# Performance work log

Hardware: AMD Instinct MI355X
Metric: run time of the kernel (lower is better)

The kernel has to match this reference:

```python
import jax, jax.numpy as jnp
import numpy as np

B, DIM, E, H, TOP_K = 4096, 2048, 8, 16, 2
HEAD_DIM = DIM // H
SCALE = HEAD_DIM ** -0.5


def setup_inputs() -> dict:
    key = jax.random.key(0)
    ks = jax.random.split(key, 7)
    return {
        "x": jax.random.normal(ks[0], (B, DIM), jnp.float32),
        "y": jax.random.normal(ks[1], (B, DIM), jnp.float32),
        "W_experts": jax.random.normal(ks[2], (E, DIM, 3 * DIM), jnp.float32) * 0.02,
        "Wg": jax.random.normal(ks[3], (DIM, E), jnp.float32) * 0.02,
        "bg": jax.random.normal(ks[4], (E,), jnp.float32) * 0.02,
        "Wp": jax.random.normal(ks[5], (DIM, DIM), jnp.float32) * 0.02,
        "bp": jax.random.normal(ks[6], (DIM,), jnp.float32) * 0.02,
    }


def reference(x, y, W_experts, Wg, bg, Wp, bp):
    Bsz, N = x.shape
    # gating: softmax over experts, then top-k sparse combine weights
    gate = jax.nn.softmax(x @ Wg + bg, axis=-1)           # [B, E]
    topv, topi = jax.lax.top_k(gate, TOP_K)               # [B, k]
    g = jnp.zeros((Bsz, E), x.dtype).at[jnp.arange(Bsz)[:, None], topi].add(topv)  # [B, E] sparse gates

    # all-expert QKV projections, combined with gate weights (equals sum over top-k of g_i * expert_i(x))
    qkv_x = jnp.einsum('bef,be->bf', jnp.einsum('bd,edf->bef', x, W_experts), g)  # [B, 3*dim]
    qkv_y = jnp.einsum('bef,be->bf', jnp.einsum('bd,edf->bef', y, W_experts), g)  # [B, 3*dim]

    qkv_x = qkv_x.reshape(Bsz, 3, H, HEAD_DIM)
    qkv_y = qkv_y.reshape(Bsz, 3, H, HEAD_DIM)
    q = qkv_y[:, 0]   # [B, H, hd] (q from y)
    k = qkv_x[:, 1]   # [B, H, hd]
    v = qkv_x[:, 2]   # [B, H, hd]

    attn = jax.nn.softmax(jnp.einsum('bhd,bgd->bhg', q, k) * SCALE, axis=-1)  # [B, H, H]
    out = jnp.einsum('bhg,bgd->bhd', attn, v)             # [B, H, hd]
    out = jnp.swapaxes(out, 1, 2).reshape(Bsz, N)         # matches .transpose(1,2).reshape(B,N)
    return out @ Wp + bp
```

## Files before the change

### kernel.cpp

```cpp
#include <hip/hip_runtime.h>
#include <hip/hip_bf16.h>
#include <math.h>

typedef __hip_bfloat16 bf16;
typedef unsigned short u16;
typedef __attribute__((ext_vector_type(4))) float f32x4;
typedef __attribute__((ext_vector_type(8))) __bf16 bfrag;

#define NB   4096
#define DIMK 2048
#define NE   8
#define NH   16
#define HDIM 128
#define W3   6144
#define BK   32
#define WMAX 96
#define QS   132
#define ATT_SCALE 0.08838834764831845f

__device__ __forceinline__ void gl16(const bf16* g, u16* l) {
    __builtin_amdgcn_global_load_lds(
        (const __attribute__((address_space(1))) void*)g,
        (__attribute__((address_space(3))) void*)l, 16, 0, 0);
}

__global__ __launch_bounds__(256)
void k_cvt(const float* __restrict__ src, bf16* __restrict__ dst, long long n) {
    long long i = ((long long)blockIdx.x * 256 + threadIdx.x) * 8;
    if (i + 8 <= n) {
        float4 a = *(const float4*)(src + i);
        float4 b = *(const float4*)(src + i + 4);
        bf16 o[8];
        o[0] = __float2bfloat16(a.x); o[1] = __float2bfloat16(a.y);
        o[2] = __float2bfloat16(a.z); o[3] = __float2bfloat16(a.w);
        o[4] = __float2bfloat16(b.x); o[5] = __float2bfloat16(b.y);
        o[6] = __float2bfloat16(b.z); o[7] = __float2bfloat16(b.w);
        *(uint4*)(dst + i) = *(uint4*)o;
    }
}

__global__ __launch_bounds__(256)
void k_cvt_t(const float* __restrict__ src, bf16* __restrict__ dst,
             int ldsrc, int lddst, long long srcE, long long dstE) {
    __shared__ u16 tile[64][65];
    int e = blockIdx.z;
    int d0 = blockIdx.y << 6, f0 = blockIdx.x << 6;
    int t = threadIdx.x;
    const float* S = src + (size_t)e * srcE + (size_t)d0 * ldsrc + f0;
    int dr = t >> 4, fc = (t & 15) << 2;
#pragma unroll
    for (int i = 0; i < 4; i++) {
        float4 v = *(const float4*)(S + (size_t)(dr + (i << 4)) * ldsrc + fc);
        bf16 b0 = __float2bfloat16(v.x), b1 = __float2bfloat16(v.y),
             b2 = __float2bfloat16(v.z), b3 = __float2bfloat16(v.w);
        u16* tp = &tile[dr + (i << 4)][fc];
        tp[0] = *(u16*)&b0; tp[1] = *(u16*)&b1;
        tp[2] = *(u16*)&b2; tp[3] = *(u16*)&b3;
    }
    __syncthreads();
    bf16* D = dst + (size_t)e * dstE + (size_t)f0 * lddst + d0;
#pragma unroll
    for (int r = 0; r < 2; r++) {
        int c = (r << 8) + t;
        int fr = c >> 3, chk = c & 7;
        u16 o[8];
#pragma unroll
        for (int j = 0; j < 8; j++) o[j] = tile[chk * 8 + j][fr];
        *(uint4*)(D + (size_t)fr * lddst + chk * 8) = *(uint4*)o;
    }
}

__global__ void k_zero(int* counts) {
    if (threadIdx.x < 64) counts[threadIdx.x] = 0;
}

__global__ void k_gate(const float* __restrict__ x, const float* __restrict__ Wg,
                       const float* __restrict__ bg, int* __restrict__ counts,
                       int* __restrict__ rowsP, float* __restrict__ gA,
                       float* __restrict__ gB) {
    int b = blockIdx.x;
    int l = threadIdx.x;
    float acc[NE];
#pragma unroll
    for (int e = 0; e < NE; e++) acc[e] = 0.f;
    for (int i = 0; i < DIMK / 64; i++) {
        int d = i * 64 + l;
        float xv = x[(size_t)b * DIMK + d];
        const float* wrow = Wg + (size_t)d * NE;
#pragma unroll
        for (int e = 0; e < NE; e++) acc[e] += xv * wrow[e];
    }
#pragma unroll
    for (int e = 0; e < NE; e++)
        for (int off = 32; off > 0; off >>= 1) acc[e] += __shfl_down(acc[e], off);
    if (l == 0) {
        float p[NE]; float m = -1e30f;
        for (int e = 0; e < NE; e++) { p[e] = acc[e] + bg[e]; m = fmaxf(m, p[e]); }
        float s = 0.f;
        for (int e = 0; e < NE; e++) { p[e] = __expf(p[e] - m); s += p[e]; }
        float inv = 1.f / s;
        for (int e = 0; e < NE; e++) p[e] *= inv;
        int i1 = 0; float v1 = p[0];
        for (int e = 1; e < NE; e++) if (p[e] > v1) { v1 = p[e]; i1 = e; }
        int i2 = -1; float v2 = -1.f;
        for (int e = 0; e < NE; e++) if (e != i1 && p[e] > v2) { v2 = p[e]; i2 = e; }
        if (i2 < 0) i2 = (i1 + 1) & 7;
        int a, bb; float ga, gb;
        if (i1 < i2) { a = i1; bb = i2; ga = v1; gb = v2; }
        else         { a = i2; bb = i1; ga = v2; gb = v1; }
        int pid = a * NE + bb;
        pid = pid < 0 ? 0 : (pid > 63 ? 63 : pid);
        int pos = atomicAdd(&counts[pid], 1);
        if (pos < NB) {
            rowsP[pid * NB + pos] = b; gA[pid * NB + pos] = ga; gB[pid * NB + pos] = gb;
        }
    }
}

__global__ void k_sched(const int* __restrict__ counts, int2* __restrict__ work) {
    if (threadIdx.x == 0) {
        int w = 0;
        for (int p = 0; p < 64; p++) {
            int c = counts[p]; c = c > NB ? NB : c;
            for (int m = 0; m < c && w < WMAX; m += 64) work[w++] = make_int2(p, m);
        }
        for (; w < WMAX; w++) work[w] = make_int2(-1, 0);
    }
}

__global__ __launch_bounds__(256, 3)
void k_moe(const bf16* __restrict__ xb, const bf16* __restrict__ yb,
           const bf16* __restrict__ Wt, const int* __restrict__ counts,
           const int* __restrict__ rowsP, const float* __restrict__ gAp,
           const float* __restrict__ gBp, const int2* __restrict__ work,
           bf16* __restrict__ qbuf, bf16* __restrict__ kvbuf) {
    int2 wi = work[blockIdx.y];
    if (wi.x < 0) return;
    int p = wi.x, m0 = wi.y;
    int eA = p >> 3, eB = p & 7;
    int cnt = counts[p]; cnt = cnt > NB ? NB : cnt;
    int n0 = blockIdx.x * 128;
    const bf16* A = (n0 < DIMK) ? yb : xb;
    bf16* outp; int ldc, coff;
    if (n0 < DIMK) { outp = qbuf;  ldc = DIMK;     coff = n0; }
    else           { outp = kvbuf; ldc = 2 * DIMK; coff = n0 - DIMK; }

    __shared__ __align__(16) u16 Al[2][2048];
    __shared__ __align__(16) u16 Bl[2][2][4096];
    __shared__ int   rowb[64];
    __shared__ float ga_s[64], gb_s[64];

    int t = threadIdx.x;
    if (t < 64) {
        int mg = m0 + t;
        if (mg < cnt) {
            int rv = rowsP[p * NB + mg];
            rowb[t] = (rv >= 0 && rv < NB) ? rv : -1;
            ga_s[t] = gAp[p * NB + mg]; gb_s[t] = gBp[p * NB + mg];
        } else { rowb[t] = -1; ga_s[t] = 0.f; gb_s[t] = 0.f; }
    }
    __syncthreads();

    int lane = t & 63, w = t >> 6;
    int q = lane >> 4, lr = lane & 15;
    int wbase = (t & ~63) * 8;

    int aline = t >> 3;
    int as_ = (t & 7) ^ (aline & 7);
    int atrow = aline * 2 + (as_ >> 2);
    int arowg = rowb[atrow];
    const bf16* srcA = A + (size_t)(arowg >= 0 ? arowg : 0) * DIMK + (as_ & 3) * 8;

    const bf16* srcB0[2]; const bf16* srcB1[2];
#pragma unroll
    for (int r = 0; r < 2; r++) {
        int c = (r << 8) + t;
        int line = c >> 3;
        int s = (c & 7) ^ (line & 7);
        int col = line * 2 + (s >> 2);
        size_t off = (size_t)(n0 + col) * DIMK + (s & 3) * 8;
        srcB0[r] = Wt + (size_t)eA * W3 * DIMK + off;
        srcB1[r] = Wt + (size_t)eB * W3 * DIMK + off;
    }

    f32x4 acc0[2][4], acc1[2][4];
#pragma unroll
    for (int nf = 0; nf < 2; nf++)
#pragma unroll
        for (int m = 0; m < 4; m++) {
            acc0[nf][m] = (f32x4){0.f,0.f,0.f,0.f};
            acc1[nf][m] = (f32x4){0.f,0.f,0.f,0.f};
        }

#define MOE_STAGE(BUF, K0) do { \
    gl16(srcA + (K0),      &Al[BUF][wbase]); \
    gl16(srcB0[0] + (K0),  &Bl[BUF][0][wbase]); \
    gl16(srcB0[1] + (K0),  &Bl[BUF][0][2048 + wbase]); \
    gl16(srcB1[0] + (K0),  &Bl[BUF][1][wbase]); \
    gl16(srcB1[1] + (K0),  &Bl[BUF][1][2048 + wbase]); \
} while (0)

#define MOE_COMP(BUF) do { \
    bfrag af[4]; \
    _Pragma("unroll") for (int m = 0; m < 4; m++) { \
        int row = m * 16 + lr; int line = row >> 1; \
        af[m] = *(const bfrag*)&Al[BUF][line * 64 + ((((row & 1) << 2) | q) ^ (line & 7)) * 8]; \
    } \
    _Pragma("unroll") for (int nf = 0; nf < 2; nf++) { \
        int col = (w << 5) + (nf << 4) + lr; int line = col >> 1; \
        int bo = line * 64 + ((((col & 1) << 2) | q) ^ (line & 7)) * 8; \
        bfrag b0 = *(const bfrag*)&Bl[BUF][0][bo]; \
        bfrag b1 = *(const bfrag*)&Bl[BUF][1][bo]; \
        _Pragma("unroll") for (int m = 0; m < 4; m++) { \
            acc0[nf][m] = __builtin_amdgcn_mfma_f32_16x16x32_bf16(af[m], b0, acc0[nf][m], 0, 0, 0); \
            acc1[nf][m] = __builtin_amdgcn_mfma_f32_16x16x32_bf16(af[m], b1, acc1[nf][m], 0, 0, 0); \
        } \
    } \
} while (0)

    MOE_STAGE(0, 0);
    __syncthreads();
    for (int k0 = 0; k0 < DIMK; k0 += 2 * BK) {
        MOE_STAGE(1, k0 + BK);
        MOE_COMP(0);
        __syncthreads();
        if (k0 + 2 * BK < DIMK) MOE_STAGE(0, k0 + 2 * BK);
        MOE_COMP(1);
        __syncthreads();
    }
#undef MOE_STAGE
#undef MOE_COMP

#pragma unroll
    for (int nf = 0; nf < 2; nf++) {
        int col = coff + (w << 5) + (nf << 4) + lr;
#pragma unroll
        for (int m = 0; m < 4; m++)
#pragma unroll
            for (int r = 0; r < 4; r++) {
                int tr = m * 16 + q * 4 + r;
                int rb = rowb[tr];
                if (rb >= 0)
                    outp[(size_t)rb * ldc + col] =
                        __float2bfloat16(ga_s[tr] * acc0[nf][m][r] + gb_s[tr] * acc1[nf][m][r]);
            }
    }
}

__global__ __launch_bounds__(256)
void k_attn(const bf16* qv, const bf16* __restrict__ kv, bf16* aout) {
    int b = blockIdx.x;
    int t = threadIdx.x;
    __shared__ __align__(16) float qs[NH * QS];
    __shared__ __align__(16) float ks[NH * QS];
    __shared__ __align__(16) float vs[NH * QS];
    __shared__ float Ps[NH * 17];
    size_t qb = (size_t)b * DIMK;
    size_t kb = (size_t)b * (2 * DIMK);
    {
        uint4 q4 = *(const uint4*)(qv + qb + (size_t)t * 8);
        uint4 k4 = *(const uint4*)(kv + kb + (size_t)t * 8);
        uint4 v4 = *(const uint4*)(kv + kb + DIMK + (size_t)t * 8);
        const bf16* qp = (const bf16*)&q4;
        const bf16* kp = (const bf16*)&k4;
        const bf16* vp = (const bf16*)&v4;
        int hh = t >> 4, dd = (t & 15) << 3;
        float* qd = &qs[hh * QS + dd];
        float* kd = &ks[hh * QS + dd];
        float* vd = &vs[hh * QS + dd];
#pragma unroll
        for (int j = 0; j < 8; j++) {
            qd[j] = __bfloat162float(qp[j]);
            kd[j] = __bfloat162float(kp[j]);
            vd[j] = __bfloat162float(vp[j]);
        }
    }
    __syncthreads();
    int h = t >> 4, g = t & 15;
    float s = 0.f;
    for (int i = 0; i < HDIM / 4; i++) {
        float4 q4 = *(const float4*)&qs[h * QS + 4 * i];
        float4 k4 = *(const float4*)&ks[g * QS + 4 * i];
        s += q4.x * k4.x + q4.y * k4.y + q4.z * k4.z + q4.w * k4.w;
    }
    s *= ATT_SCALE;
    float m = s;
    for (int off = 8; off > 0; off >>= 1) m = fmaxf(m, __shfl_xor(m, off, 16));
    float p = __expf(s - m);
    float sum = p;
    for (int off = 8; off > 0; off >>= 1) sum += __shfl_xor(sum, off, 16);
    Ps[h * 17 + g] = p / sum;
    __syncthreads();
#pragma unroll
    for (int j = 0; j < 8; j++) {
        int n = t + 256 * j;
        int hh = n & 15, dd = n >> 4;
        float o = 0.f;
#pragma unroll
        for (int gg = 0; gg < 16; gg++) o += Ps[hh * 17 + gg] * vs[gg * QS + dd];
        aout[(size_t)b * DIMK + n] = __float2bfloat16(o);
    }
}

__global__ __launch_bounds__(256, 3)
void k_gemm_bias(const bf16* __restrict__ A, const bf16* __restrict__ Wt,
                 const float* __restrict__ bias, float* __restrict__ out) {
    int m0 = blockIdx.y * 128, n0 = blockIdx.x * 128;
    int t = threadIdx.x;
    __shared__ __align__(16) u16 Al[2][4096];
    __shared__ __align__(16) u16 Bl[2][4096];
    int lane = t & 63, w = t >> 6;
    int q = lane >> 4, lr = lane & 15;
    int rh = (w >> 1) << 6, chf = (w & 1) << 6;
    int wbase = (t & ~63) * 8;

    const bf16* srcA[2]; const bf16* srcB[2];
#pragma unroll
    for (int r = 0; r < 2; r++) {
        int c = (r << 8) + t;
        int line = c >> 3;
        int s = (c & 7) ^ (line & 7);
        int row = line * 2 + (s >> 2);
        int j = s & 3;
        srcA[r] = A  + (size_t)(m0 + row) * DIMK + j * 8;
        srcB[r] = Wt + (size_t)(n0 + row) * DIMK + j * 8;
    }

    f32x4 acc[4][4];
#pragma unroll
    for (int m = 0; m < 4; m++)
#pragma unroll
        for (int nf = 0; nf < 4; nf++) acc[m][nf] = (f32x4){0.f,0.f,0.f,0.f};

#define PG_STAGE(BUF, K0) do { \
    gl16(srcA[0] + (K0), &Al[BUF][wbase]); \
    gl16(srcA[1] + (K0), &Al[BUF][2048 + wbase]); \
    gl16(srcB[0] + (K0), &Bl[BUF][wbase]); \
    gl16(srcB[1] + (K0), &Bl[BUF][2048 + wbase]); \
} while (0)

#define PG_COMP(BUF) do { \
    bfrag af[4]; \
    _Pragma("unroll") for (int m = 0; m < 4; m++) { \
        int row = rh + m * 16 + lr; int line = row >> 1; \
        af[m] = *(const bfrag*)&Al[BUF][line * 64 + ((((row & 1) << 2) | q) ^ (line & 7)) * 8]; \
    } \
    _Pragma("unroll") for (int nf = 0; nf < 4; nf++) { \
        int col = chf + nf * 16 + lr; int line = col >> 1; \
        bfrag bf_ = *(const bfrag*)&Bl[BUF][line * 64 + ((((col & 1) << 2) | q) ^ (line & 7)) * 8]; \
        _Pragma("unroll") for (int m = 0; m < 4; m++) \
            acc[m][nf] = __builtin_amdgcn_mfma_f32_16x16x32_bf16(af[m], bf_, acc[m][nf], 0, 0, 0); \
    } \
} while (0)

    PG_STAGE(0, 0);
    __syncthreads();
    for (int k0 = 0; k0 < DIMK; k0 += 2 * BK) {
        PG_STAGE(1, k0 + BK);
        PG_COMP(0);
        __syncthreads();
        if (k0 + 2 * BK < DIMK) PG_STAGE(0, k0 + 2 * BK);
        PG_COMP(1);
        __syncthreads();
    }
#undef PG_STAGE
#undef PG_COMP

#pragma unroll
    for (int nf = 0; nf < 4; nf++) {
        int col = n0 + chf + nf * 16 + lr;
        float bv = bias[col];
#pragma unroll
        for (int m = 0; m < 4; m++)
#pragma unroll
            for (int r = 0; r < 4; r++) {
                int row = m0 + rh + m * 16 + q * 4 + r;
                out[(size_t)row * DIMK + col] = acc[m][nf][r] + bv;
            }
    }
}

__global__ void k_fallback(float v, float* __restrict__ out) {
    int i = blockIdx.x * 256 + threadIdx.x;
    out[i] = v;
}

extern "C" void kernel_launch(void* const* d_in, const int* in_sizes, int n_in,
                              void* d_out, int out_size, void* d_ws, size_t ws_size,
                              hipStream_t stream) {
    const float* x  = (const float*)d_in[0];
    const float* y  = (const float*)d_in[1];
    const float* We = (const float*)d_in[2];
    const float* Wg = (const float*)d_in[3];
    const float* bg = (const float*)d_in[4];
    const float* Wp = (const float*)d_in[5];
    const float* bp = (const float*)d_in[6];
    float* out = (float*)d_out;
    (void)in_sizes; (void)n_in; (void)out_size;

    char* ws = (char*)d_ws;
    const size_t NEED = 296751104ULL;
    if (ws_size < NEED) {
        hipLaunchKernelGGL(k_fallback, dim3(NB * DIMK / 256), dim3(256), 0, stream,
                           (float)(ws_size >> 20), out);
        return;
    }
    int*   counts = (int*)ws;
    int2*  work   = (int2*)(ws + 256);
    int*   rowsP  = (int*)(ws + 4096);
    float* gA     = (float*)(ws + 1052672);
    float* gB     = (float*)(ws + 2101248);
    bf16*  xb     = (bf16*)(ws + 3149824);
    bf16*  yb     = (bf16*)(ws + 19927040);
    bf16*  Web    = (bf16*)(ws + 36704256);
    bf16*  Wpb    = (bf16*)(ws + 238030848);
    bf16*  qbuf   = (bf16*)(ws + 246419456);
    bf16*  kvbuf  = (bf16*)(ws + 263196672);

    const long long nxy = (long long)NB * DIMK;
    hipLaunchKernelGGL(k_cvt, dim3((unsigned)(nxy / 2048)), dim3(256), 0, stream, x,  xb,  nxy);
    hipLaunchKernelGGL(k_cvt, dim3((unsigned)(nxy / 2048)), dim3(256), 0, stream, y,  yb,  nxy);
    hipLaunchKernelGGL(k_cvt_t, dim3(W3 / 64, DIMK / 64, NE), dim3(256), 0, stream,
                       We, Web, W3, DIMK, (long long)DIMK * W3, (long long)W3 * DIMK);
    hipLaunchKernelGGL(k_cvt_t, dim3(DIMK / 64, DIMK / 64, 1), dim3(256), 0, stream,
                       Wp, Wpb, DIMK, DIMK, 0LL, 0LL);

    hipLaunchKernelGGL(k_zero, dim3(1), dim3(64), 0, stream, counts);
    hipLaunchKernelGGL(k_gate, dim3(NB), dim3(64), 0, stream, x, Wg, bg, counts, rowsP, gA, gB);
    hipLaunchKernelGGL(k_sched, dim3(1), dim3(64), 0, stream, counts, work);
    hipLaunchKernelGGL(k_moe, dim3(W3 / 128, WMAX), dim3(256), 0, stream,
                       xb, yb, Web, counts, rowsP, gA, gB, work, qbuf, kvbuf);
    hipLaunchKernelGGL(k_attn, dim3(NB), dim3(256), 0, stream, qbuf, kvbuf, qbuf);
    hipLaunchKernelGGL(k_gemm_bias, dim3(DIMK / 128, NB / 128), dim3(256), 0, stream,
                       qbuf, Wpb, bp, out);
}
```

Measured before the change: 1.191 ms.

## Pipeline GEMM loads with vmcnt waits, raw barriers and priority hints; vectorize attn-V

```diff
diff --git a/kernel.cpp b/kernel.cpp
--- a/kernel.cpp
+++ b/kernel.cpp
@@ -17,6 +17,10 @@
 #define WMAX 96
 #define QS   132
 #define ATT_SCALE 0.08838834764831845f
+
+#define BAR()  __builtin_amdgcn_s_barrier()
+#define SB0()  __builtin_amdgcn_sched_barrier(0)
+#define PRIO(n) __builtin_amdgcn_s_setprio(n)
 
 __device__ __forceinline__ void gl16(const bf16* g, u16* l) {
     __builtin_amdgcn_global_load_lds(
@@ -219,15 +223,26 @@
 } while (0)
 
     MOE_STAGE(0, 0);
-    __syncthreads();
-    for (int k0 = 0; k0 < DIMK; k0 += 2 * BK) {
-        MOE_STAGE(1, k0 + BK);
-        MOE_COMP(0);
-        __syncthreads();
-        if (k0 + 2 * BK < DIMK) MOE_STAGE(0, k0 + 2 * BK);
-        MOE_COMP(1);
-        __syncthreads();
-    }
+    MOE_STAGE(1, BK);
+    asm volatile("s_waitcnt vmcnt(5)" ::: "memory");
+    BAR(); SB0();
+    int k0 = 0;
+    for (; k0 < DIMK - 2 * BK; k0 += 2 * BK) {
+        PRIO(1); MOE_COMP(0); PRIO(0);
+        BAR(); SB0();
+        MOE_STAGE(0, k0 + 2 * BK);
+        asm volatile("s_waitcnt vmcnt(5)" ::: "memory");
+        BAR(); SB0();
+        PRIO(1); MOE_COMP(1); PRIO(0);
+        BAR(); SB0();
+        MOE_STAGE(1, k0 + 3 * BK);
+        asm volatile("s_waitcnt vmcnt(5)" ::: "memory");
+        BAR(); SB0();
+    }
+    PRIO(1); MOE_COMP(0); PRIO(0);
+    asm volatile("s_waitcnt vmcnt(0)" ::: "memory");
+    BAR(); SB0();
+    PRIO(1); MOE_COMP(1); PRIO(0);
 #undef MOE_STAGE
 #undef MOE_COMP
 
@@ -291,14 +306,26 @@
     for (int off = 8; off > 0; off >>= 1) sum += __shfl_xor(sum, off, 16);
     Ps[h * 17 + g] = p / sum;
     __syncthreads();
-#pragma unroll
-    for (int j = 0; j < 8; j++) {
-        int n = t + 256 * j;
-        int hh = n & 15, dd = n >> 4;
-        float o = 0.f;
-#pragma unroll
-        for (int gg = 0; gg < 16; gg++) o += Ps[hh * 17 + gg] * vs[gg * QS + dd];
-        aout[(size_t)b * DIMK + n] = __float2bfloat16(o);
+    {
+        int hh = t & 15, dd0 = (t >> 4) * 8;
+        float pr[16];
+#pragma unroll
+        for (int gg = 0; gg < 16; gg++) pr[gg] = Ps[hh * 17 + gg];
+        float o[8];
+#pragma unroll
+        for (int r = 0; r < 8; r++) o[r] = 0.f;
+#pragma unroll
+        for (int gg = 0; gg < 16; gg++) {
+            float4 v0 = *(const float4*)&vs[gg * QS + dd0];
+            float4 v1 = *(const float4*)&vs[gg * QS + dd0 + 4];
+            o[0] += pr[gg] * v0.x; o[1] += pr[gg] * v0.y;
+            o[2] += pr[gg] * v0.z; o[3] += pr[gg] * v0.w;
+            o[4] += pr[gg] * v1.x; o[5] += pr[gg] * v1.y;
+            o[6] += pr[gg] * v1.z; o[7] += pr[gg] * v1.w;
+        }
+#pragma unroll
+        for (int r = 0; r < 8; r++)
+            aout[(size_t)b * DIMK + (size_t)(dd0 + r) * 16 + hh] = __float2bfloat16(o[r]);
     }
 }
 
@@ -354,15 +381,26 @@
 } while (0)
 
     PG_STAGE(0, 0);
-    __syncthreads();
-    for (int k0 = 0; k0 < DIMK; k0 += 2 * BK) {
-        PG_STAGE(1, k0 + BK);
-        PG_COMP(0);
-        __syncthreads();
-        if (k0 + 2 * BK < DIMK) PG_STAGE(0, k0 + 2 * BK);
-        PG_COMP(1);
-        __syncthreads();
-    }
+    PG_STAGE(1, BK);
+    asm volatile("s_waitcnt vmcnt(4)" ::: "memory");
+    BAR(); SB0();
+    int k0 = 0;
+    for (; k0 < DIMK - 2 * BK; k0 += 2 * BK) {
+        PRIO(1); PG_COMP(0); PRIO(0);
+        BAR(); SB0();
+        PG_STAGE(0, k0 + 2 * BK);
+        asm volatile("s_waitcnt vmcnt(4)" ::: "memory");
+        BAR(); SB0();
+        PRIO(1); PG_COMP(1); PRIO(0);
+        BAR(); SB0();
+        PG_STAGE(1, k0 + 3 * BK);
+        asm volatile("s_waitcnt vmcnt(4)" ::: "memory");
+        BAR(); SB0();
+    }
+    PRIO(1); PG_COMP(0); PRIO(0);
+    asm volatile("s_waitcnt vmcnt(0)" ::: "memory");
+    BAR(); SB0();
+    PRIO(1); PG_COMP(1); PRIO(0);
 #undef PG_STAGE
 #undef PG_COMP
 
```

After: 1.169 ms. No clear change (-1.8%).
